# Kernel tuning notes

Hardware: AMD Instinct MI355X
Metric: run time of the kernel (lower is better)

Reference implementation:

```python
import jax, jax.numpy as jnp
import numpy as np

N_NODES = 50000
N_EDGES = 800000
HIDDEN = 256
LAYERS = 10


def setup_inputs() -> dict:
    key = jax.random.key(0)
    ks = jax.random.split(key, 8)
    x = jax.random.normal(ks[0], (N_NODES, 1), dtype=jnp.float32)
    edge_index = jax.random.randint(ks[1], (2, N_EDGES), 0, N_NODES, dtype=jnp.int64)
    # GCNConv weights (Glorot-ish scale)
    W1 = jax.random.normal(ks[2], (1, HIDDEN), dtype=jnp.float32) * (1.0 / np.sqrt(1))
    b1 = jnp.zeros((HIDDEN,), dtype=jnp.float32)
    W = jax.random.normal(ks[3], (HIDDEN, HIDDEN), dtype=jnp.float32) * (1.0 / np.sqrt(HIDDEN))
    b = jnp.zeros((HIDDEN,), dtype=jnp.float32)
    Wc = jax.random.normal(ks[4], (HIDDEN, 1), dtype=jnp.float32) * (1.0 / np.sqrt(HIDDEN))
    bc = jnp.zeros((1,), dtype=jnp.float32)
    return {"x": x, "edge_index": edge_index, "W1": W1, "b1": b1,
            "W": W, "b": b, "Wc": Wc, "bc": bc}


def _gcn_norm(edge_index, n_nodes):
    # PyG GCNConv default: add self-loops, symmetric normalization
    loop = jnp.arange(n_nodes, dtype=edge_index.dtype)
    src = jnp.concatenate([edge_index[0], loop])
    dst = jnp.concatenate([edge_index[1], loop])
    ones = jnp.ones(src.shape[0], dtype=jnp.float32)
    deg = jax.ops.segment_sum(ones, dst, num_segments=n_nodes)
    dinv = jnp.where(deg > 0, jax.lax.rsqrt(deg), 0.0)
    norm = dinv[src] * dinv[dst]  # [E+N]
    return src, dst, norm


def _gcn_conv(h, W, b, src, dst, norm, n_nodes):
    h = h @ W                                   # [N, H] dense transform first (small GEMM)
    msg = h[src] * norm[:, None]                # gather + scale  [E+N, H]
    out = jax.ops.segment_sum(msg, dst, num_segments=n_nodes)  # scatter-add
    return out + b


def reference(x, edge_index, W1, b1, W, b, Wc, bc):
    n = x.shape[0]
    src, dst, norm = _gcn_norm(edge_index, n)  # graph is static across layers
    h = jax.nn.relu(_gcn_conv(x, W1, b1, src, dst, norm, n))
    for _ in range(1, LAYERS):  # layers 1..9 share the same weights (self.conv reused)
        h = jax.nn.relu(_gcn_conv(h, W, b, src, dst, norm, n))
    return h @ Wc + bc  # [N, 1]
```

## Files before the change

### kernel.cpp

```cpp
#include <hip/hip_runtime.h>

typedef long long ll;
typedef __attribute__((ext_vector_type(8))) short short8;
typedef __attribute__((ext_vector_type(4))) float f32x4;
constexpr int HID = 256;
constexpr int LDSS = 264;

__device__ inline ushort f2bf(float f){
  uint u = __float_as_uint(f);
  u += 0x7FFFu + ((u >> 16) & 1u);
  return (ushort)(u >> 16);
}

__global__ void k_diag(float* out, int n, float val){
  int i = blockIdx.x*256 + threadIdx.x;
  if (i < n) out[i] = val;
}

__global__ void k_detect(const int* ei, int* flag){
  __shared__ int bad;
  if (threadIdx.x == 0) bad = 0;
  __syncthreads();
  for (int i = threadIdx.x; i < 2048; i += 256)
    if (ei[2*i+1] != 0) bad = 1;
  __syncthreads();
  if (threadIdx.x == 0) *flag = bad ? 0 : 1;
}

__global__ void k_count(const int* ei, ll E, const int* flag, int* cnt){
  ll i = (ll)blockIdx.x*256 + threadIdx.x;
  if (i >= E) return;
  int f = *flag;
  int d = f ? (int)((const ll*)ei)[E + i] : ei[E + i];
  atomicAdd(&cnt[d], 1);
}

__global__ void k_scan_a(const int* __restrict__ cnt, int* __restrict__ bsum, int n){
  __shared__ int s[256];
  int t = threadIdx.x, i = blockIdx.x*256 + t;
  s[t] = (i < n) ? cnt[i] : 0;
  __syncthreads();
  for (int off = 128; off; off >>= 1){
    if (t < off) s[t] += s[t + off];
    __syncthreads();
  }
  if (t == 0) bsum[blockIdx.x] = s[0];
}

__global__ void k_scan_b(const int* __restrict__ bsum, int* __restrict__ boff,
                         int nb, int* __restrict__ row_ptr, int n){
  __shared__ int s[256];
  int t = threadIdx.x;
  int v = (t < nb) ? bsum[t] : 0;
  s[t] = v; __syncthreads();
  for (int off = 1; off < 256; off <<= 1){
    int add = (t >= off) ? s[t - off] : 0;
    __syncthreads();
    s[t] += add;
    __syncthreads();
  }
  if (t < nb) boff[t] = s[t] - v;
  if (t == nb - 1) row_ptr[n] = s[t];
}

__global__ void k_scan_c(const int* __restrict__ cnt, const int* __restrict__ boff,
                         int* __restrict__ row_ptr, int n){
  __shared__ int s[256];
  int t = threadIdx.x, i = blockIdx.x*256 + t;
  int v = (i < n) ? cnt[i] : 0;
  s[t] = v; __syncthreads();
  for (int off = 1; off < 256; off <<= 1){
    int add = (t >= off) ? s[t - off] : 0;
    __syncthreads();
    s[t] += add;
    __syncthreads();
  }
  if (i < n) row_ptr[i] = boff[blockIdx.x] + s[t] - v;
}

__global__ void k_dinv(const int* cnt, const float* x, float* dinv, float* xd, int n){
  int i = blockIdx.x*256 + threadIdx.x;
  if (i >= n) return;
  float dv = 1.0f / sqrtf((float)(cnt[i] + 1));
  dinv[i] = dv;
  xd[i] = x[i] * dv;
}

__global__ void k_place(const int* ei, ll E, const int* flag, int* fill, int* col){
  ll i = (ll)blockIdx.x*256 + threadIdx.x;
  if (i >= E) return;
  int f = *flag;
  int s, d;
  if (f){ const ll* e64 = (const ll*)ei; s = (int)e64[i]; d = (int)e64[E + i]; }
  else  { s = ei[i]; d = ei[E + i]; }
  int p = atomicAdd(&fill[d], 1);
  col[p] = s;
}

__global__ void k_layer1(const float* __restrict__ xd, const int* __restrict__ row_ptr,
                         const int* __restrict__ col, float* __restrict__ g, int n){
  int i = blockIdx.x*256 + threadIdx.x;
  if (i >= n) return;
  float s = xd[i];
  int e0 = row_ptr[i], e1 = row_ptr[i+1];
  for (int e = e0; e < e1; ++e) s += xd[col[e]];
  g[i] = s;
}

__global__ void k_splitW(const float* __restrict__ W, short* __restrict__ Bt){
  int idx = blockIdx.x*256 + threadIdx.x;
  if (idx >= 16*8*64) return;
  int nb = idx >> 9, kc = (idx >> 6) & 7, l = idx & 63;
  short8 hi, lo;
  #pragma unroll
  for (int j = 0; j < 8; ++j){
    int k = kc*32 + ((l >> 4) * 8) + j;
    int c = nb*16 + (l & 15);
    float wv = W[k*HID + c];
    ushort h = f2bf(wv);
    float hf = __uint_as_float((uint)h << 16);
    hi[j] = (short)h;
    lo[j] = (short)f2bf(wv - hf);
  }
  ((short8*)Bt)[idx] = hi;
  ((short8*)Bt)[8192 + idx] = lo;
}

template<int MODE>
__global__ __launch_bounds__(256, 2) void k_gemm_mfma(
  const float* __restrict__ Ain, const short* __restrict__ Bt,
  const float* __restrict__ bias, const float* __restrict__ W1,
  const float* __restrict__ dinv, ushort* __restrict__ ts_bf, int n)
{
  __shared__ short Ah[64*LDSS];
  __shared__ short Al[64*LDSS];
  int t = threadIdx.x;
  int r0 = blockIdx.x * 64;

  #pragma unroll
  for (int i = 0; i < 8; ++i){
    int id  = i*256 + t;
    int row = id >> 5;
    int c16 = id & 31;
    int v   = r0 + row;
    short8 hi8 = {0,0,0,0,0,0,0,0}, lo8 = {0,0,0,0,0,0,0,0};
    if (v < n){
      float dv = dinv[v];
      float vals[8];
      if (MODE == 0){
        float gv = dv * Ain[v];
        const float4* wp = (const float4*)(W1 + c16*8);
        const float4* bp = (const float4*)(bias + c16*8);
        float4 w0 = wp[0], w1 = wp[1], b0 = bp[0], b1 = bp[1];
        vals[0]=fmaf(gv,w0.x,b0.x); vals[1]=fmaf(gv,w0.y,b0.y);
        vals[2]=fmaf(gv,w0.z,b0.z); vals[3]=fmaf(gv,w0.w,b0.w);
        vals[4]=fmaf(gv,w1.x,b1.x); vals[5]=fmaf(gv,w1.y,b1.y);
        vals[6]=fmaf(gv,w1.z,b1.z); vals[7]=fmaf(gv,w1.w,b1.w);
      } else {
        const float4* ap = (const float4*)(Ain + (size_t)v*HID + c16*8);
        const float4* bp = (const float4*)(bias + c16*8);
        float4 a0 = ap[0], a1 = ap[1], b0 = bp[0], b1 = bp[1];
        vals[0]=fmaf(dv,a0.x,b0.x); vals[1]=fmaf(dv,a0.y,b0.y);
        vals[2]=fmaf(dv,a0.z,b0.z); vals[3]=fmaf(dv,a0.w,b0.w);
        vals[4]=fmaf(dv,a1.x,b1.x); vals[5]=fmaf(dv,a1.y,b1.y);
        vals[6]=fmaf(dv,a1.z,b1.z); vals[7]=fmaf(dv,a1.w,b1.w);
      }
      #pragma unroll
      for (int j = 0; j < 8; ++j){
        float a = fmaxf(vals[j], 0.f);
        ushort h = f2bf(a);
        float hf = __uint_as_float((uint)h << 16);
        hi8[j] = (short)h;
        lo8[j] = (short)f2bf(a - hf);
      }
    }
    int off = row*LDSS + c16*8;
    *(short8*)&Ah[off] = hi8;
    *(short8*)&Al[off] = lo8;
  }
  __syncthreads();

  int l = t & 63, w = t >> 6;
  const short8* Btv = (const short8*)Bt;
  f32x4 acc[4][4];
  #pragma unroll
  for (int m = 0; m < 4; ++m)
    #pragma unroll
    for (int nf = 0; nf < 4; ++nf)
      acc[m][nf] = (f32x4){0.f,0.f,0.f,0.f};

  for (int kc = 0; kc < 8; ++kc){
    short8 ah[4], al[4];
    #pragma unroll
    for (int m = 0; m < 4; ++m){
      int row = m*16 + (l & 15);
      int off = row*LDSS + (kc*4 + (l >> 4))*8;
      ah[m] = *(const short8*)&Ah[off];
      al[m] = *(const short8*)&Al[off];
    }
    #pragma unroll
    for (int nf = 0; nf < 4; ++nf){
      int nb = w*4 + nf;
      short8 bh = Btv[(size_t)(nb*8 + kc)*64 + l];
      short8 bl = Btv[(size_t)8192 + (nb*8 + kc)*64 + l];
      #pragma unroll
      for (int m = 0; m < 4; ++m){
        acc[m][nf] = __builtin_amdgcn_mfma_f32_16x16x32_bf16(ah[m], bh, acc[m][nf], 0,0,0);
        acc[m][nf] = __builtin_amdgcn_mfma_f32_16x16x32_bf16(al[m], bh, acc[m][nf], 0,0,0);
        acc[m][nf] = __builtin_amdgcn_mfma_f32_16x16x32_bf16(ah[m], bl, acc[m][nf], 0,0,0);
      }
    }
  }

  #pragma unroll
  for (int m = 0; m < 4; ++m){
    int rowb = r0 + m*16 + ((l >> 4)*4);
    #pragma unroll
    for (int r = 0; r < 4; ++r){
      int v = rowb + r;
      if (v < n){
        float dv = dinv[v];
        #pragma unroll
        for (int nf = 0; nf < 4; ++nf){
          int colb = w*64 + nf*16 + (l & 15);
          ts_bf[(size_t)v*HID + colb] = f2bf(dv * acc[m][nf][r]);
        }
      }
    }
  }
}

__device__ inline void bfacc(uint2 u, float4& a){
  a.x += __uint_as_float(u.x << 16);
  a.y += __uint_as_float(u.x & 0xFFFF0000u);
  a.z += __uint_as_float(u.y << 16);
  a.w += __uint_as_float(u.y & 0xFFFF0000u);
}

__global__ __launch_bounds__(256, 4) void k_scatter_bf(
  const ushort* __restrict__ ts_bf, const int* __restrict__ row_ptr,
  const int* __restrict__ col, float* __restrict__ acc, int n)
{
  int w = (int)((blockIdx.x*256 + threadIdx.x) >> 6);
  int lane = threadIdx.x & 63;
  if (w >= n) return;
  const uint2* tsp = ((const uint2*)ts_bf) + lane;
  int e0 = row_ptr[w], e1 = row_ptr[w+1];

  float4 a0 = make_float4(0.f,0.f,0.f,0.f);
  float4 a1 = make_float4(0.f,0.f,0.f,0.f);
  float4 a2 = make_float4(0.f,0.f,0.f,0.f);
  float4 a3 = make_float4(0.f,0.f,0.f,0.f);
  bfacc(tsp[(size_t)w*64], a0);

  int e = e0;
  for (; e + 4 <= e1; e += 4){
    int c0 = col[e+0], c1 = col[e+1], c2 = col[e+2], c3 = col[e+3];
    uint2 v0 = tsp[(size_t)c0*64];
    uint2 v1 = tsp[(size_t)c1*64];
    uint2 v2 = tsp[(size_t)c2*64];
    uint2 v3 = tsp[(size_t)c3*64];
    bfacc(v0, a0); bfacc(v1, a1); bfacc(v2, a2); bfacc(v3, a3);
  }
  for (; e < e1; ++e){
    uint2 v = tsp[(size_t)col[e]*64];
    bfacc(v, a0);
  }

  a0.x += a1.x + a2.x + a3.x;
  a0.y += a1.y + a2.y + a3.y;
  a0.z += a1.z + a2.z + a3.z;
  a0.w += a1.w + a2.w + a3.w;
  ((float4*)acc)[(size_t)w*64 + lane] = a0;
}

__global__ __launch_bounds__(256) void k_out(
  const float* __restrict__ acc, const float* __restrict__ bias,
  const float* __restrict__ Wc, const float* __restrict__ bc,
  const float* __restrict__ dinv, float* __restrict__ out, int n)
{
  int w = (int)((blockIdx.x*256 + threadIdx.x) >> 6);
  int lane = threadIdx.x & 63;
  if (w >= n) return;
  float dv = dinv[w];
  float4 a  = ((const float4*)acc)[(size_t)w*64 + lane];
  float4 bb = ((const float4*)bias)[lane];
  float4 wc = ((const float4*)Wc)[lane];
  float s = fmaxf(fmaf(dv, a.x, bb.x), 0.f)*wc.x
          + fmaxf(fmaf(dv, a.y, bb.y), 0.f)*wc.y
          + fmaxf(fmaf(dv, a.z, bb.z), 0.f)*wc.z
          + fmaxf(fmaf(dv, a.w, bb.w), 0.f)*wc.w;
  #pragma unroll
  for (int off = 32; off; off >>= 1) s += __shfl_down(s, off, 64);
  if (lane == 0) out[w] = s + bc[0];
}

extern "C" void kernel_launch(void* const* d_in, const int* in_sizes, int n_in,
                              void* d_out, int out_size, void* d_ws, size_t ws_size,
                              hipStream_t stream)
{
  const float* x  = (const float*)d_in[0];
  const int*   ei = (const int*)d_in[1];
  const float* W1 = (const float*)d_in[2];
  const float* b1 = (const float*)d_in[3];
  const float* Wm = (const float*)d_in[4];
  const float* bm = (const float*)d_in[5];
  const float* Wc = (const float*)d_in[6];
  const float* bc = (const float*)d_in[7];
  float* out = (float*)d_out;
  const int N = in_sizes[0];
  const ll  E = in_sizes[1] / 2;

  char* ws = (char*)d_ws;
  size_t off = 0;
  auto carve = [&](size_t bytes)->char*{
    char* p = ws + off; off += (bytes + 255) & ~(size_t)255; return p;
  };
  int*   cnt     = (int*)  carve((size_t)N*4);
  int*   row_ptr = (int*)  carve((size_t)(N+1)*4);
  int*   fill    = (int*)  carve((size_t)N*4);
  float* dinv    = (float*)carve((size_t)N*4);
  float* xd      = (float*)carve((size_t)N*4);
  float* g       = (float*)carve((size_t)N*4);
  int*   flag    = (int*)  carve(256);
  int*   bsum    = (int*)  carve(1024);
  int*   boff    = (int*)  carve(1024);
  short* Bt      = (short*)carve((size_t)2*8192*8*2);
  int*   col     = (int*)  carve((size_t)E*4);
  ushort* ts_bf  = (ushort*)carve((size_t)N*HID*2);
  float* acc     = (float*)carve((size_t)N*HID*4);
  if (off > ws_size){
    k_diag<<<(out_size+255)/256, 256, 0, stream>>>(out, out_size, (float)(ws_size >> 20));
    return;
  }

  hipMemsetAsync(cnt, 0, (size_t)N*4, stream);
  k_detect<<<1, 256, 0, stream>>>(ei, flag);
  int eblocks = (int)((E + 255) / 256);
  k_count<<<eblocks, 256, 0, stream>>>(ei, E, flag, cnt);
  int nb = (N + 255) / 256;
  k_scan_a<<<nb, 256, 0, stream>>>(cnt, bsum, N);
  k_scan_b<<<1, 256, 0, stream>>>(bsum, boff, nb, row_ptr, N);
  k_scan_c<<<nb, 256, 0, stream>>>(cnt, boff, row_ptr, N);
  k_dinv<<<(N+255)/256, 256, 0, stream>>>(cnt, x, dinv, xd, N);
  hipMemcpyAsync(fill, row_ptr, (size_t)N*4, hipMemcpyDeviceToDevice, stream);
  k_place<<<eblocks, 256, 0, stream>>>(ei, E, flag, fill, col);
  k_splitW<<<32, 256, 0, stream>>>(Wm, Bt);
  k_layer1<<<(N+255)/256, 256, 0, stream>>>(xd, row_ptr, col, g, N);

  int gblocks = (N + 63) / 64;
  int sblocks = (N + 3) / 4;
  k_gemm_mfma<0><<<gblocks, 256, 0, stream>>>(g, Bt, b1, W1, dinv, ts_bf, N);
  k_scatter_bf<<<sblocks, 256, 0, stream>>>(ts_bf, row_ptr, col, acc, N);
  for (int l = 0; l < 8; ++l){
    k_gemm_mfma<1><<<gblocks, 256, 0, stream>>>(acc, Bt, bm, nullptr, dinv, ts_bf, N);
    k_scatter_bf<<<sblocks, 256, 0, stream>>>(ts_bf, row_ptr, col, acc, N);
  }
  k_out<<<sblocks, 256, 0, stream>>>(acc, bm, Wc, bc, dinv, out, N);
}
```

Measured before the change: 1.025 ms.

## Store activations as bf16 and fuse bias/ReLU epilogue into scatter kernel

The scatter kernel now applies the dinv scale, bias and ReLU itself and writes bf16 activations instead of an fp32 accumulator. The GEMM then loads bf16 rows directly, drops the low-part A split (one of three MFMAs per step) and halves its LDS use, which allows a higher occupancy launch bound. The aim is to halve activation memory traffic and cut GEMM compute and conversion work. The cost is precision: activations are now rounded to bf16 between layers, where before they kept a near-fp32 split.

```diff
diff --git a/kernel.cpp b/kernel.cpp
--- a/kernel.cpp
+++ b/kernel.cpp
@@ -127,13 +127,12 @@
 }
 
 template<int MODE>
-__global__ __launch_bounds__(256, 2) void k_gemm_mfma(
-  const float* __restrict__ Ain, const short* __restrict__ Bt,
+__global__ __launch_bounds__(256, 4) void k_gemm_mfma(
+  const void* __restrict__ Ain, const short* __restrict__ Bt,
   const float* __restrict__ bias, const float* __restrict__ W1,
   const float* __restrict__ dinv, ushort* __restrict__ ts_bf, int n)
 {
   __shared__ short Ah[64*LDSS];
-  __shared__ short Al[64*LDSS];
   int t = threadIdx.x;
   int r0 = blockIdx.x * 64;
 
@@ -143,40 +142,26 @@
     int row = id >> 5;
     int c16 = id & 31;
     int v   = r0 + row;
-    short8 hi8 = {0,0,0,0,0,0,0,0}, lo8 = {0,0,0,0,0,0,0,0};
+    short8 hi8 = {0,0,0,0,0,0,0,0};
     if (v < n){
-      float dv = dinv[v];
-      float vals[8];
       if (MODE == 0){
-        float gv = dv * Ain[v];
+        float gv = dinv[v] * ((const float*)Ain)[v];
         const float4* wp = (const float4*)(W1 + c16*8);
         const float4* bp = (const float4*)(bias + c16*8);
         float4 w0 = wp[0], w1 = wp[1], b0 = bp[0], b1 = bp[1];
-        vals[0]=fmaf(gv,w0.x,b0.x); vals[1]=fmaf(gv,w0.y,b0.y);
-        vals[2]=fmaf(gv,w0.z,b0.z); vals[3]=fmaf(gv,w0.w,b0.w);
-        vals[4]=fmaf(gv,w1.x,b1.x); vals[5]=fmaf(gv,w1.y,b1.y);
-        vals[6]=fmaf(gv,w1.z,b1.z); vals[7]=fmaf(gv,w1.w,b1.w);
+        hi8[0] = (short)f2bf(fmaxf(fmaf(gv,w0.x,b0.x), 0.f));
+        hi8[1] = (short)f2bf(fmaxf(fmaf(gv,w0.y,b0.y), 0.f));
+        hi8[2] = (short)f2bf(fmaxf(fmaf(gv,w0.z,b0.z), 0.f));
+        hi8[3] = (short)f2bf(fmaxf(fmaf(gv,w0.w,b0.w), 0.f));
+        hi8[4] = (short)f2bf(fmaxf(fmaf(gv,w1.x,b1.x), 0.f));
+        hi8[5] = (short)f2bf(fmaxf(fmaf(gv,w1.y,b1.y), 0.f));
+        hi8[6] = (short)f2bf(fmaxf(fmaf(gv,w1.z,b1.z), 0.f));
+        hi8[7] = (short)f2bf(fmaxf(fmaf(gv,w1.w,b1.w), 0.f));
       } else {
-        const float4* ap = (const float4*)(Ain + (size_t)v*HID + c16*8);
-        const float4* bp = (const float4*)(bias + c16*8);
-        float4 a0 = ap[0], a1 = ap[1], b0 = bp[0], b1 = bp[1];
-        vals[0]=fmaf(dv,a0.x,b0.x); vals[1]=fmaf(dv,a0.y,b0.y);
-        vals[2]=fmaf(dv,a0.z,b0.z); vals[3]=fmaf(dv,a0.w,b0.w);
-        vals[4]=fmaf(dv,a1.x,b1.x); vals[5]=fmaf(dv,a1.y,b1.y);
-        vals[6]=fmaf(dv,a1.z,b1.z); vals[7]=fmaf(dv,a1.w,b1.w);
-      }
-      #pragma unroll
-      for (int j = 0; j < 8; ++j){
-        float a = fmaxf(vals[j], 0.f);
-        ushort h = f2bf(a);
-        float hf = __uint_as_float((uint)h << 16);
-        hi8[j] = (short)h;
-        lo8[j] = (short)f2bf(a - hf);
+        hi8 = ((const short8*)Ain)[(size_t)v*32 + c16];
       }
     }
-    int off = row*LDSS + c16*8;
-    *(short8*)&Ah[off] = hi8;
-    *(short8*)&Al[off] = lo8;
+    *(short8*)&Ah[row*LDSS + c16*8] = hi8;
   }
   __syncthreads();
 
@@ -190,13 +175,11 @@
       acc[m][nf] = (f32x4){0.f,0.f,0.f,0.f};
 
   for (int kc = 0; kc < 8; ++kc){
-    short8 ah[4], al[4];
+    short8 ah[4];
     #pragma unroll
     for (int m = 0; m < 4; ++m){
       int row = m*16 + (l & 15);
-      int off = row*LDSS + (kc*4 + (l >> 4))*8;
-      ah[m] = *(const short8*)&Ah[off];
-      al[m] = *(const short8*)&Al[off];
+      ah[m] = *(const short8*)&Ah[row*LDSS + (kc*4 + (l >> 4))*8];
     }
     #pragma unroll
     for (int nf = 0; nf < 4; ++nf){
@@ -206,7 +189,6 @@
       #pragma unroll
       for (int m = 0; m < 4; ++m){
         acc[m][nf] = __builtin_amdgcn_mfma_f32_16x16x32_bf16(ah[m], bh, acc[m][nf], 0,0,0);
-        acc[m][nf] = __builtin_amdgcn_mfma_f32_16x16x32_bf16(al[m], bh, acc[m][nf], 0,0,0);
         acc[m][nf] = __builtin_amdgcn_mfma_f32_16x16x32_bf16(ah[m], bl, acc[m][nf], 0,0,0);
       }
     }
@@ -239,7 +221,8 @@
 
 __global__ __launch_bounds__(256, 4) void k_scatter_bf(
   const ushort* __restrict__ ts_bf, const int* __restrict__ row_ptr,
-  const int* __restrict__ col, float* __restrict__ acc, int n)
+  const int* __restrict__ col, const float* __restrict__ bias,
+  const float* __restrict__ dinv, ushort* __restrict__ Abf, int n)
 {
   int w = (int)((blockIdx.x*256 + threadIdx.x) >> 6);
   int lane = threadIdx.x & 63;
@@ -271,25 +254,30 @@
   a0.y += a1.y + a2.y + a3.y;
   a0.z += a1.z + a2.z + a3.z;
   a0.w += a1.w + a2.w + a3.w;
-  ((float4*)acc)[(size_t)w*64 + lane] = a0;
+
+  float dv = dinv[w];
+  float4 bb = ((const float4*)bias)[lane];
+  uint2 o;
+  o.x = (uint)f2bf(fmaxf(fmaf(dv, a0.x, bb.x), 0.f))
+      | ((uint)f2bf(fmaxf(fmaf(dv, a0.y, bb.y), 0.f)) << 16);
+  o.y = (uint)f2bf(fmaxf(fmaf(dv, a0.z, bb.z), 0.f))
+      | ((uint)f2bf(fmaxf(fmaf(dv, a0.w, bb.w), 0.f)) << 16);
+  ((uint2*)Abf)[(size_t)w*64 + lane] = o;
 }
 
 __global__ __launch_bounds__(256) void k_out(
-  const float* __restrict__ acc, const float* __restrict__ bias,
-  const float* __restrict__ Wc, const float* __restrict__ bc,
-  const float* __restrict__ dinv, float* __restrict__ out, int n)
+  const ushort* __restrict__ Abf, const float* __restrict__ Wc,
+  const float* __restrict__ bc, float* __restrict__ out, int n)
 {
   int w = (int)((blockIdx.x*256 + threadIdx.x) >> 6);
   int lane = threadIdx.x & 63;
   if (w >= n) return;
-  float dv = dinv[w];
-  float4 a  = ((const float4*)acc)[(size_t)w*64 + lane];
-  float4 bb = ((const float4*)bias)[lane];
+  uint2 u = ((const uint2*)Abf)[(size_t)w*64 + lane];
   float4 wc = ((const float4*)Wc)[lane];
-  float s = fmaxf(fmaf(dv, a.x, bb.x), 0.f)*wc.x
-          + fmaxf(fmaf(dv, a.y, bb.y), 0.f)*wc.y
-          + fmaxf(fmaf(dv, a.z, bb.z), 0.f)*wc.z
-          + fmaxf(fmaf(dv, a.w, bb.w), 0.f)*wc.w;
+  float s = __uint_as_float(u.x << 16)          * wc.x
+          + __uint_as_float(u.x & 0xFFFF0000u)  * wc.y
+          + __uint_as_float(u.y << 16)          * wc.z
+          + __uint_as_float(u.y & 0xFFFF0000u)  * wc.w;
   #pragma unroll
   for (int off = 32; off; off >>= 1) s += __shfl_down(s, off, 64);
   if (lane == 0) out[w] = s + bc[0];
@@ -328,7 +316,7 @@
   short* Bt      = (short*)carve((size_t)2*8192*8*2);
   int*   col     = (int*)  carve((size_t)E*4);
   ushort* ts_bf  = (ushort*)carve((size_t)N*HID*2);
-  float* acc     = (float*)carve((size_t)N*HID*4);
+  ushort* Abf    = (ushort*)carve((size_t)N*HID*2);
   if (off > ws_size){
     k_diag<<<(out_size+255)/256, 256, 0, stream>>>(out, out_size, (float)(ws_size >> 20));
     return;
@@ -351,10 +339,10 @@
   int gblocks = (N + 63) / 64;
   int sblocks = (N + 3) / 4;
   k_gemm_mfma<0><<<gblocks, 256, 0, stream>>>(g, Bt, b1, W1, dinv, ts_bf, N);
-  k_scatter_bf<<<sblocks, 256, 0, stream>>>(ts_bf, row_ptr, col, acc, N);
+  k_scatter_bf<<<sblocks, 256, 0, stream>>>(ts_bf, row_ptr, col, bm, dinv, Abf, N);
   for (int l = 0; l < 8; ++l){
-    k_gemm_mfma<1><<<gblocks, 256, 0, stream>>>(acc, Bt, bm, nullptr, dinv, ts_bf, N);
-    k_scatter_bf<<<sblocks, 256, 0, stream>>>(ts_bf, row_ptr, col, acc, N);
-  }
-  k_out<<<sblocks, 256, 0, stream>>>(acc, bm, Wc, bc, dinv, out, N);
-}
+    k_gemm_mfma<1><<<gblocks, 256, 0, stream>>>(Abf, Bt, bm, nullptr, dinv, ts_bf, N);
+    k_scatter_bf<<<sblocks, 256, 0, stream>>>(ts_bf, row_ptr, col, bm, dinv, Abf, N);
+  }
+  k_out<<<sblocks, 256, 0, stream>>>(Abf, Wc, bc, out, N);
+}
```

After: 868.1 us. 15.3% less time.
